# Optimization experiments

Hardware: AMD Instinct MI355X
Metric: run time of the kernel (lower is better)

Reference implementation:

```python
import jax, jax.numpy as jnp
import numpy as np

B, T, I, R, O = 1, 2048, 8, 4096, 8
SPECTRAL_RADIUS = 0.9
SPARSITY = 0.1


def setup_inputs() -> dict:
    key = jax.random.key(0)
    k1, k2, k3, k4, k5, k6 = jax.random.split(key, 6)
    x = jax.random.normal(k1, (B, T, I), dtype=jnp.float32)
    Win = jax.random.normal(k2, (R, I), dtype=jnp.float32)
    W = jax.random.normal(k3, (R, R), dtype=jnp.float32)
    # sparse mask + spectral-radius scaling (circular-law approx: rho(sparse gaussian) ~ sqrt(sparsity*R))
    mask = (jax.random.uniform(k4, (R, R)) < SPARSITY).astype(jnp.float32)
    W = W * mask * (SPECTRAL_RADIUS / jnp.sqrt(SPARSITY * R))
    Wout_w = jax.random.normal(k5, (O, R), dtype=jnp.float32) / jnp.sqrt(R)
    Wout_b = jax.random.normal(k6, (O,), dtype=jnp.float32) * 0.01
    return {"x": x, "Win": Win, "W": W, "Wout_w": Wout_w, "Wout_b": Wout_b}


def reference(x, Win, W, Wout_w, Wout_b):
    Bb = x.shape[0]
    h0 = jnp.zeros((Bb, W.shape[0]), dtype=x.dtype)

    def step(h, xt):  # xt: [B, I]
        h = jnp.tanh(xt @ Win.T + h @ W.T)          # [B, R]
        out = h @ Wout_w.T + Wout_b                  # [B, O]
        return h, out

    xs = jnp.swapaxes(x, 0, 1)                       # [T, B, I]
    _, outs = jax.lax.scan(step, h0, xs)             # outs: [T, B, O]
    return jnp.swapaxes(outs, 0, 1)                  # [B, T, O]
```

## Files before the change

kernel.cpp:

```cpp
#include <hip/hip_runtime.h>
#include <math.h>


#define T_STEPS 2048
#define R_DIM   4096
#define I_DIM   8
#define O_DIM   8
#define NWG     64
#define ROWS_PER_WG (R_DIM / NWG)
#define HALF_ROWS 32
#define POOL_CAP 16384
#define BLOCK    1024
#define NS       36

typedef float v4f __attribute__((ext_vector_type(4)));

__device__ float        g_hist[(size_t)T_STEPS * R_DIM];
__device__ unsigned int g_flag[NWG * 32];

__global__ void esn_init_kernel() {
    for (int i = threadIdx.x; i < NWG * 32; i += blockDim.x)
        __hip_atomic_store(&g_flag[i], 0u, __ATOMIC_RELAXED,
                           __HIP_MEMORY_SCOPE_SYSTEM);
}

__launch_bounds__(BLOCK, 1)
__global__ void esn_recur_kernel(const float* __restrict__ x,
                                 const float* __restrict__ Win,
                                 const float* __restrict__ W) {
    __shared__ uint2 s_pool[POOL_CAP];
    __shared__ float s_h[R_DIM];
    __shared__ int   s_start[HALF_ROWS + 1];
    __shared__ int   s_cnt[HALF_ROWS];
    __shared__ float s_win[ROWS_PER_WG][I_DIM];

    const int wg   = blockIdx.x;
    const int tid  = threadIdx.x;
    const int lane = tid & 63;
    const int wave = tid >> 6;
    const int row0 = wg * ROWS_PER_WG;

    const int row16 = tid >> 4;
    const int sub   = tid & 15;

    float    rv[NS];
    unsigned ri[NS / 2];

    for (int pass = 0; pass < 2; ++pass) {
        const int prow0 = row0 + pass * HALF_ROWS;
        for (int rr = wave; rr < HALF_ROWS; rr += 16) {
            const float* wrow = W + (size_t)(prow0 + rr) * R_DIM;
            int cnt = 0;
            for (int base = 0; base < R_DIM; base += 64) {
                float v = wrow[base + lane];
                cnt += __popcll(__ballot(v != 0.0f));
            }
            if (lane == 0) s_cnt[rr] = cnt;
        }
        __syncthreads();
        if (tid == 0) {
            int acc = 0;
            for (int rr = 0; rr < HALF_ROWS; ++rr) {
                s_start[rr] = (acc < POOL_CAP) ? acc : POOL_CAP;
                acc += s_cnt[rr];
            }
            s_start[HALF_ROWS] = (acc < POOL_CAP) ? acc : POOL_CAP;
        }
        __syncthreads();
        for (int rr = wave; rr < HALF_ROWS; rr += 16) {
            const float* wrow = W + (size_t)(prow0 + rr) * R_DIM;
            int off = s_start[rr];
            for (int base = 0; base < R_DIM; base += 64) {
                float v = wrow[base + lane];
                unsigned long long m = __ballot(v != 0.0f);
                int pre = __popcll(m & ((1ull << lane) - 1ull));
                if (v != 0.0f) {
                    int pos = off + pre;
                    if (pos < POOL_CAP) {
                        s_pool[pos].x = __float_as_uint(v);
                        s_pool[pos].y = (base + lane) * 4;
                    }
                }
                off += __popcll(m);
            }
        }
        __syncthreads();
        const int lr = row16 - pass * HALF_ROWS;
        if (lr >= 0 && lr < HALF_ROWS) {
            const int st = s_start[lr];
            const int en = s_start[lr + 1];
            #pragma unroll
            for (int m = 0; m < NS; ++m) {
                const int e = st + sub + (m << 4);
                float    v = 0.0f;
                unsigned b = 0u;
                if (e < en) { uint2 p = s_pool[e]; v = __uint_as_float(p.x); b = p.y; }
                rv[m] = v;
                if ((m & 1) == 0) ri[m >> 1] = b;
                else              ri[m >> 1] |= (b << 16);
            }
        }
        __syncthreads();
    }
    if (tid < ROWS_PER_WG * I_DIM) {
        int rr = tid / I_DIM, c = tid % I_DIM;
        s_win[rr][c] = Win[(size_t)(row0 + rr) * I_DIM + c];
    }
    __syncthreads();

    const unsigned* fsrc = &g_flag[(tid >> 4) << 5];

    for (int t = 0; t < T_STEPS; ++t) {
        const float4* xp = (const float4*)(x + (size_t)t * I_DIM);
        const float4 xa = xp[0];
        const float4 xb = xp[1];

        if (t > 0) {
            const unsigned need = (unsigned)t << 4;
            const float* hp = g_hist + (size_t)(t - 1) * R_DIM
                              + (size_t)tid * 4;
            v4f r0; unsigned fv;
            for (;;) {
                asm volatile(
                    "global_load_dwordx4 %0, %2, off sc0 sc1\n\t"
                    "global_load_dword %1, %3, off sc0 sc1\n\t"
                    "s_waitcnt vmcnt(0)"
                    : "=v"(r0), "=v"(fv)
                    : "v"(hp), "v"(fsrc)
                    : "memory");
                if (__all(fv >= need)) break;
                __builtin_amdgcn_s_sleep(2);
            }
            *(v4f*)(s_h + (size_t)tid * 4) = r0;
            __syncthreads();
        }

        float acc = 0.0f;
        if (t > 0) {
            #pragma unroll
            for (int m = 0; m < NS; ++m) {
                const unsigned ba = (m & 1) ? (ri[m >> 1] >> 16)
                                            : (ri[m >> 1] & 0xffffu);
                const float hv = *(const float*)((const char*)s_h + ba);
                acc += rv[m] * hv;
            }
        }
        acc += __shfl_xor(acc, 8, 16);
        acc += __shfl_xor(acc, 4, 16);
        acc += __shfl_xor(acc, 2, 16);
        acc += __shfl_xor(acc, 1, 16);

        if (sub == 0) {
            float a = acc;
            a += s_win[row16][0] * xa.x;
            a += s_win[row16][1] * xa.y;
            a += s_win[row16][2] * xa.z;
            a += s_win[row16][3] * xa.w;
            a += s_win[row16][4] * xb.x;
            a += s_win[row16][5] * xb.y;
            a += s_win[row16][6] * xb.z;
            a += s_win[row16][7] * xb.w;
            float h = tanhf(a);
            __hip_atomic_store(&g_hist[(size_t)t * R_DIM + row0 + row16], h,
                               __ATOMIC_RELAXED, __HIP_MEMORY_SCOPE_SYSTEM);
        }
        asm volatile("s_waitcnt vmcnt(0)" ::: "memory");
        if (lane == 0)
            (void)__hip_atomic_fetch_add(&g_flag[wg << 5], 1u,
                                         __ATOMIC_RELAXED,
                                         __HIP_MEMORY_SCOPE_SYSTEM);
        __syncthreads();
    }
}

__global__ void esn_out_kernel(const float* __restrict__ Wout_w,
                               const float* __restrict__ Wout_b,
                               float* __restrict__ out) {
    const int t = blockIdx.x;
    const int lane = threadIdx.x;
    const float* hp = g_hist + (size_t)t * R_DIM;
    float acc[O_DIM];
    #pragma unroll
    for (int o = 0; o < O_DIM; ++o) acc[o] = 0.0f;
    for (int i = lane; i < R_DIM; i += 256) {
        float h0 = __hip_atomic_load(hp + i,       __ATOMIC_RELAXED, __HIP_MEMORY_SCOPE_SYSTEM);
        float h1 = __hip_atomic_load(hp + i + 64,  __ATOMIC_RELAXED, __HIP_MEMORY_SCOPE_SYSTEM);
        float h2 = __hip_atomic_load(hp + i + 128, __ATOMIC_RELAXED, __HIP_MEMORY_SCOPE_SYSTEM);
        float h3 = __hip_atomic_load(hp + i + 192, __ATOMIC_RELAXED, __HIP_MEMORY_SCOPE_SYSTEM);
        #pragma unroll
        for (int o = 0; o < O_DIM; ++o) acc[o] += h0 * Wout_w[(size_t)o * R_DIM + i];
        #pragma unroll
        for (int o = 0; o < O_DIM; ++o) acc[o] += h1 * Wout_w[(size_t)o * R_DIM + i + 64];
        #pragma unroll
        for (int o = 0; o < O_DIM; ++o) acc[o] += h2 * Wout_w[(size_t)o * R_DIM + i + 128];
        #pragma unroll
        for (int o = 0; o < O_DIM; ++o) acc[o] += h3 * Wout_w[(size_t)o * R_DIM + i + 192];
    }
    #pragma unroll
    for (int o = 0; o < O_DIM; ++o) {
        float a = acc[o];
        a += __shfl_xor(a, 32);
        a += __shfl_xor(a, 16);
        a += __shfl_xor(a, 8);
        a += __shfl_xor(a, 4);
        a += __shfl_xor(a, 2);
        a += __shfl_xor(a, 1);
        if (lane == 0) out[(size_t)t * O_DIM + o] = a + Wout_b[o];
    }
}

extern "C" void kernel_launch(void* const* d_in, const int* in_sizes, int n_in,
                              void* d_out, int out_size, void* d_ws, size_t ws_size,
                              hipStream_t stream) {
    const float* x    = (const float*)d_in[0];
    const float* Win  = (const float*)d_in[1];
    const float* W    = (const float*)d_in[2];
    const float* Ww   = (const float*)d_in[3];
    const float* Wb   = (const float*)d_in[4];
    float* out = (float*)d_out;

    hipLaunchKernelGGL(esn_init_kernel, dim3(1), dim3(256), 0, stream);

    void* args[] = { (void*)&x, (void*)&Win, (void*)&W };
    hipLaunchCooperativeKernel((void*)esn_recur_kernel, dim3(NWG), dim3(BLOCK),
                               args, 0, stream);

    hipLaunchKernelGGL(esn_out_kernel, dim3(T_STEPS), dim3(64), 0, stream,
                       Ww, Wb, out);
}
```

Measured before the change: 8.340 ms.

## Replace flag counters with tagged per-workgroup mailboxes for hidden-state exchange

Each workgroup no longer polls shared per-workgroup counter flags followed by a separate history load. It now polls its own double-buffered mailbox, where every hidden value is packed with an epoch and step tag into a 64-bit word written by the producer. This folds the data and its readiness signal into one load, removes the wait-for-store-then-atomic-increment handshake on the producer side, and uses an epoch counter so the mailboxes never need clearing. The cost is 64x fan-out writes per step (each workgroup writes its 64 values to all 64 mailboxes) and double-width loads for the consumer.

```diff
diff --git a/kernel.cpp b/kernel.cpp
--- a/kernel.cpp
+++ b/kernel.cpp
@@ -12,16 +12,22 @@
 #define POOL_CAP 16384
 #define BLOCK    1024
 #define NS       36
+#define TAG_MUL  4096
 
 typedef float v4f __attribute__((ext_vector_type(4)));
-
-__device__ float        g_hist[(size_t)T_STEPS * R_DIM];
-__device__ unsigned int g_flag[NWG * 32];
+typedef unsigned int v4u __attribute__((ext_vector_type(4)));
+
+__device__ unsigned long long g_mail[2][NWG][R_DIM];
+__device__ float              g_hist[(size_t)T_STEPS * R_DIM];
+__device__ unsigned int       g_epoch;
 
 __global__ void esn_init_kernel() {
-    for (int i = threadIdx.x; i < NWG * 32; i += blockDim.x)
-        __hip_atomic_store(&g_flag[i], 0u, __ATOMIC_RELAXED,
+    if (threadIdx.x == 0) {
+        unsigned e = __hip_atomic_load(&g_epoch, __ATOMIC_RELAXED,
+                                       __HIP_MEMORY_SCOPE_SYSTEM) + 1u;
+        __hip_atomic_store(&g_epoch, e, __ATOMIC_RELAXED,
                            __HIP_MEMORY_SCOPE_SYSTEM);
+    }
 }
 
 __launch_bounds__(BLOCK, 1)
@@ -30,6 +36,7 @@
                                  const float* __restrict__ W) {
     __shared__ uint2 s_pool[POOL_CAP];
     __shared__ float s_h[R_DIM];
+    __shared__ float s_hout[ROWS_PER_WG];
     __shared__ int   s_start[HALF_ROWS + 1];
     __shared__ int   s_cnt[HALF_ROWS];
     __shared__ float s_win[ROWS_PER_WG][I_DIM];
@@ -45,6 +52,10 @@
 
     float    rv[NS];
     unsigned ri[NS / 2];
+
+    const unsigned tag_base =
+        __hip_atomic_load(&g_epoch, __ATOMIC_RELAXED,
+                          __HIP_MEMORY_SCOPE_SYSTEM) * TAG_MUL;
 
     for (int pass = 0; pass < 2; ++pass) {
         const int prow0 = row0 + pass * HALF_ROWS;
@@ -108,7 +119,8 @@
     }
     __syncthreads();
 
-    const unsigned* fsrc = &g_flag[(tid >> 4) << 5];
+    const int fan_c  = tid >> 4;
+    const int fan_r4 = (tid & 15) << 2;
 
     for (int t = 0; t < T_STEPS; ++t) {
         const float4* xp = (const float4*)(x + (size_t)t * I_DIM);
@@ -116,22 +128,29 @@
         const float4 xb = xp[1];
 
         if (t > 0) {
-            const unsigned need = (unsigned)t << 4;
-            const float* hp = g_hist + (size_t)(t - 1) * R_DIM
-                              + (size_t)tid * 4;
-            v4f r0; unsigned fv;
-            for (;;) {
+            const unsigned exp_tag = tag_base + (unsigned)t;
+            const unsigned long long* mp =
+                &g_mail[(t - 1) & 1][wg][(size_t)tid * 4];
+            v4u q0, q1;
+            bool ok;
+            do {
                 asm volatile(
                     "global_load_dwordx4 %0, %2, off sc0 sc1\n\t"
-                    "global_load_dword %1, %3, off sc0 sc1\n\t"
+                    "global_load_dwordx4 %1, %2, off offset:16 sc0 sc1\n\t"
                     "s_waitcnt vmcnt(0)"
-                    : "=v"(r0), "=v"(fv)
-                    : "v"(hp), "v"(fsrc)
+                    : "=v"(q0), "=v"(q1)
+                    : "v"(mp)
                     : "memory");
-                if (__all(fv >= need)) break;
-                __builtin_amdgcn_s_sleep(2);
-            }
-            *(v4f*)(s_h + (size_t)tid * 4) = r0;
+                ok = (q0.y == exp_tag) & (q0.w == exp_tag) &
+                     (q1.y == exp_tag) & (q1.w == exp_tag);
+                if (!ok) __builtin_amdgcn_s_sleep(1);
+            } while (!ok);
+            v4f hv;
+            hv.x = __uint_as_float(q0.x);
+            hv.y = __uint_as_float(q0.z);
+            hv.z = __uint_as_float(q1.x);
+            hv.w = __uint_as_float(q1.z);
+            *(v4f*)(s_h + (size_t)tid * 4) = hv;
             __syncthreads();
         }
 
@@ -141,8 +160,8 @@
             for (int m = 0; m < NS; ++m) {
                 const unsigned ba = (m & 1) ? (ri[m >> 1] >> 16)
                                             : (ri[m >> 1] & 0xffffu);
-                const float hv = *(const float*)((const char*)s_h + ba);
-                acc += rv[m] * hv;
+                const float hvv = *(const float*)((const char*)s_h + ba);
+                acc += rv[m] * hvv;
             }
         }
         acc += __shfl_xor(acc, 8, 16);
@@ -161,15 +180,26 @@
             a += s_win[row16][6] * xb.z;
             a += s_win[row16][7] * xb.w;
             float h = tanhf(a);
-            __hip_atomic_store(&g_hist[(size_t)t * R_DIM + row0 + row16], h,
-                               __ATOMIC_RELAXED, __HIP_MEMORY_SCOPE_SYSTEM);
-        }
-        asm volatile("s_waitcnt vmcnt(0)" ::: "memory");
-        if (lane == 0)
-            (void)__hip_atomic_fetch_add(&g_flag[wg << 5], 1u,
-                                         __ATOMIC_RELAXED,
-                                         __HIP_MEMORY_SCOPE_SYSTEM);
-        __syncthreads();
+            s_hout[row16] = h;
+            g_hist[(size_t)t * R_DIM + row0 + row16] = h;
+        }
+        __syncthreads();
+
+        {
+            const unsigned long long tg =
+                (unsigned long long)(tag_base + (unsigned)(t + 1)) << 32;
+            const float4 hq = *(const float4*)&s_hout[fan_r4];
+            unsigned long long* dst =
+                &g_mail[t & 1][fan_c][(size_t)(row0 + fan_r4)];
+            __hip_atomic_store(dst + 0, tg | __float_as_uint(hq.x),
+                               __ATOMIC_RELAXED, __HIP_MEMORY_SCOPE_SYSTEM);
+            __hip_atomic_store(dst + 1, tg | __float_as_uint(hq.y),
+                               __ATOMIC_RELAXED, __HIP_MEMORY_SCOPE_SYSTEM);
+            __hip_atomic_store(dst + 2, tg | __float_as_uint(hq.z),
+                               __ATOMIC_RELAXED, __HIP_MEMORY_SCOPE_SYSTEM);
+            __hip_atomic_store(dst + 3, tg | __float_as_uint(hq.w),
+                               __ATOMIC_RELAXED, __HIP_MEMORY_SCOPE_SYSTEM);
+        }
     }
 }
 
@@ -219,7 +249,7 @@
     const float* Wb   = (const float*)d_in[4];
     float* out = (float*)d_out;
 
-    hipLaunchKernelGGL(esn_init_kernel, dim3(1), dim3(256), 0, stream);
+    hipLaunchKernelGGL(esn_init_kernel, dim3(1), dim3(64), 0, stream);
 
     void* args[] = { (void*)&x, (void*)&Win, (void*)&W };
     hipLaunchCooperativeKernel((void*)esn_recur_kernel, dim3(NWG), dim3(BLOCK),
```

New measurement: 13.74 ms. 1.65x slower.
